# Performance work log

Measured on AMD Instinct MI355X. Metric: run time of the kernel, lower is better.

Reference implementation:

```python
import jax, jax.numpy as jnp
import numpy as np

DIM = 1024
HEADS = 16
MLP = 4096

def setup_inputs() -> dict:
    key = jax.random.key(0)
    ks = jax.random.split(key, 8)
    s = 0.02
    return {
        "x": jax.random.normal(ks[0], (4, 2048, DIM), dtype=jnp.float32),
        "W_qkv": jax.random.normal(ks[1], (DIM, 3 * DIM), dtype=jnp.float32) * s,
        "W_o": jax.random.normal(ks[2], (DIM, DIM), dtype=jnp.float32) * s,
        "b_o": jnp.zeros((DIM,), dtype=jnp.float32),
        "g1": jnp.ones((DIM,), dtype=jnp.float32),
        "be1": jnp.zeros((DIM,), dtype=jnp.float32),
        "W1": jax.random.normal(ks[3], (DIM, MLP), dtype=jnp.float32) * s,
        "b1": jnp.zeros((MLP,), dtype=jnp.float32),
        "W2": jax.random.normal(ks[4], (MLP, DIM), dtype=jnp.float32) * s,
        "b2": jnp.zeros((DIM,), dtype=jnp.float32),
        "g2": jnp.ones((DIM,), dtype=jnp.float32),
        "be2": jnp.zeros((DIM,), dtype=jnp.float32),
    }

def _gelu(x):
    # GELU approx used in source: x * sigmoid(1.702 * x)
    return x * jax.nn.sigmoid(1.702 * x)

def _layernorm(x, g, b, eps=1e-5):
    mu = jnp.mean(x, axis=-1, keepdims=True)
    var = jnp.var(x, axis=-1, keepdims=True)
    return (x - mu) * jax.lax.rsqrt(var + eps) * g + b

def reference(x, W_qkv, W_o, b_o, g1, be1, W1, b1, W2, b2, g2, be2):
    b, n, d = x.shape
    h = HEADS
    hd = d // h
    scale = hd ** -0.5
    qkv = x @ W_qkv                               # [b,n,3d]
    q, k, v = jnp.split(qkv, 3, axis=-1)
    q = q.reshape(b, n, h, hd).transpose(0, 2, 1, 3)  # [b,h,n,hd]
    k = k.reshape(b, n, h, hd).transpose(0, 2, 1, 3)
    v = v.reshape(b, n, h, hd).transpose(0, 2, 1, 3)
    dots = jnp.einsum('bhid,bhjd->bhij', q, k) * scale  # [b,h,n,n]
    attn = jax.nn.softmax(dots, axis=-1)
    out = jnp.einsum('bhij,bhjd->bhid', attn, v)
    out = out.transpose(0, 2, 1, 3).reshape(b, n, d)
    out = out @ W_o + b_o
    x = _layernorm(x + out, g1, be1)
    ff = _gelu(x @ W1 + b1) @ W2 + b2
    x = _layernorm(x + ff, g2, be2)
    return x
```

## Files before the change

kernel.cpp:

```cpp
#include <hip/hip_runtime.h>

typedef unsigned short u16;
typedef __attribute__((ext_vector_type(4))) float f32x4;
typedef __attribute__((ext_vector_type(8))) __bf16 bf16x8;
typedef __attribute__((ext_vector_type(8))) unsigned short u16x8;
typedef __attribute__((ext_vector_type(4))) unsigned short u16x4;

__device__ __forceinline__ u16 f2bf(float f) {
  __bf16 h = (__bf16)f;
  union { __bf16 h; u16 u; } v; v.h = h;
  return v.u;
}

__device__ __forceinline__ void async16(const void* g, void* l) {
  __builtin_amdgcn_global_load_lds(
      (const __attribute__((address_space(1))) unsigned int*)g,
      (__attribute__((address_space(3))) unsigned int*)l, 16, 0, 0);
}

__device__ __forceinline__ void barrier_f() {
  asm volatile("" ::: "memory");
  __builtin_amdgcn_s_barrier();
  asm volatile("" ::: "memory");
}

__global__ __launch_bounds__(256) void cvt_f32_bf16(const float* __restrict__ in,
                                                    u16* __restrict__ out, int n4) {
  int i = blockIdx.x * 256 + threadIdx.x;
  if (i >= n4) return;
  f32x4 v = *(const f32x4*)(in + (long)i * 4);
  u16x4 o;
#pragma unroll
  for (int j = 0; j < 4; j++) o[j] = f2bf(v[j]);
  *(u16x4*)(out + (long)i * 4) = o;
}

__global__ __launch_bounds__(256) void transpose_cvt(const float* __restrict__ W,
                                                     u16* __restrict__ Wt, int K, int N) {
  __shared__ float tile[32][33];
  int n0 = blockIdx.x * 32, k0 = blockIdx.y * 32;
  int tx = threadIdx.x & 31, ty = threadIdx.x >> 5;
#pragma unroll
  for (int i = 0; i < 32; i += 8)
    tile[ty + i][tx] = W[(long)(k0 + ty + i) * N + n0 + tx];
  __syncthreads();
#pragma unroll
  for (int i = 0; i < 32; i += 8)
    Wt[(long)(n0 + ty + i) * K + k0 + tx] = f2bf(tile[tx][ty + i]);
}

__global__ __launch_bounds__(256) void vtrans(const u16* __restrict__ qkv,
                                              u16* __restrict__ vt) {
  const int bh = blockIdx.y, kt = blockIdx.x * 64;
  const int b = bh >> 4, h = bh & 15;
  const long tok0 = (long)b * 2048;
  const int t = threadIdx.x;
  const int r = t >> 3, c8 = (t & 7) * 8;
  u16x8 v0 = *(const u16x8*)&qkv[(tok0 + kt + r) * 3072 + 2048 + h * 64 + c8];
  u16x8 v1 = *(const u16x8*)&qkv[(tok0 + kt + r + 32) * 3072 + 2048 + h * 64 + c8];
#pragma unroll
  for (int j = 0; j < 8; j++) {
    vt[((long)bh * 64 + c8 + j) * 2048 + kt + r] = v0[j];
    vt[((long)bh * 64 + c8 + j) * 2048 + kt + r + 32] = v1[j];
  }
}

template <int BIAS, int GELU, int OBF, int QSCALE>
__global__ __launch_bounds__(512, 1) void gemm8p(const u16* __restrict__ A,
                                                 const u16* __restrict__ Bt,
                                                 void* __restrict__ Cp,
                                                 const float* __restrict__ bias,
                                                 int M, int N, int K) {
  __shared__ u16 As[2][256 * 64];
  __shared__ u16 Bs[2][256 * 64];
  const int t = threadIdx.x, wid = t >> 6, ln = t & 63;
  const int lr = ln & 15, lg = ln >> 4;
  const int wr = wid >> 2, wc = wid & 3;

  const int nwg = gridDim.x * gridDim.y;
  const int flat = blockIdx.y * gridDim.x + blockIdx.x;
  const int cpx = nwg >> 3;
  const int swz = (flat & 7) * cpx + (flat >> 3);
  const int m0 = (swz / gridDim.x) * 256, n0 = (swz % gridDim.x) * 256;
  const int NT = K >> 6;

  const int srow = t >> 3;
  const int sch = ((t & 7) ^ (srow & 7)) * 8;
  const u16* gA = A + (long)(m0 + srow) * K + sch;
  const u16* gB = Bt + (long)(n0 + srow) * K + sch;
  const long KL = K;

#define STAGE_A(tt, h)                                                     \
  {                                                                        \
    const u16* s_ = gA + (long)((h) * 128) * KL + (long)(tt) * 64;         \
    char* d_ = (char*)As + ((tt) & 1) * 32768 + (h) * 16384 + wid * 1024;  \
    async16(s_, d_);                                                       \
    async16(s_ + 64 * KL, d_ + 8192);                                      \
  }
#define STAGE_B(tt, h)                                                     \
  {                                                                        \
    const u16* s_ = gB + (long)((h) * 128) * KL + (long)(tt) * 64;         \
    char* d_ = (char*)Bs + ((tt) & 1) * 32768 + (h) * 16384 + wid * 1024;  \
    async16(s_, d_);                                                       \
    async16(s_ + 64 * KL, d_ + 8192);                                      \
  }

  f32x4 acc[8][4] = {};
  const int cx0 = (lg ^ (lr & 7)) * 16;
  const int cx1 = ((4 + lg) ^ (lr & 7)) * 16;

  STAGE_A(0, 0); STAGE_A(0, 1);
  STAGE_B(0, 0); STAGE_B(0, 1);
  STAGE_A(1, 0); STAGE_A(1, 1);

  for (int tK = 0; tK < NT; ++tK) {
    const int cur = tK & 1;
    const char* ldsA = (const char*)As + cur * 32768;
    const char* ldsB = (const char*)Bs + cur * 32768;
    if (tK == NT - 1) {
      asm volatile("s_waitcnt vmcnt(0)" ::: "memory");
    } else {
      asm volatile("s_waitcnt vmcnt(4)" ::: "memory");
    }
    barrier_f();

    bf16x8 aLo[4][2], aHi[4][2], bLo[2][2], bHi[2][2];
#pragma unroll
    for (int mf = 0; mf < 4; mf++) {
      int row = wr * 128 + mf * 16 + lr;
      aLo[mf][0] = *(const bf16x8*)(ldsA + row * 128 + cx0);
      aLo[mf][1] = *(const bf16x8*)(ldsA + row * 128 + cx1);
    }
#pragma unroll
    for (int nf = 0; nf < 2; nf++) {
      int row = wc * 64 + nf * 16 + lr;
      bLo[nf][0] = *(const bf16x8*)(ldsB + row * 128 + cx0);
      bLo[nf][1] = *(const bf16x8*)(ldsB + row * 128 + cx1);
    }
    if (tK + 1 < NT) STAGE_B(tK + 1, 0);
    barrier_f();
    __builtin_amdgcn_s_setprio(1);
#pragma unroll
    for (int mf = 0; mf < 4; mf++)
#pragma unroll
      for (int nf = 0; nf < 2; nf++) {
        acc[mf][nf] = __builtin_amdgcn_mfma_f32_16x16x32_bf16(aLo[mf][0], bLo[nf][0], acc[mf][nf], 0, 0, 0);
        acc[mf][nf] = __builtin_amdgcn_mfma_f32_16x16x32_bf16(aLo[mf][1], bLo[nf][1], acc[mf][nf], 0, 0, 0);
      }
    __builtin_amdgcn_s_setprio(0);
    barrier_f();

#pragma unroll
    for (int mf = 0; mf < 4; mf++) {
      int row = wr * 128 + (mf + 4) * 16 + lr;
      aHi[mf][0] = *(const bf16x8*)(ldsA + row * 128 + cx0);
      aHi[mf][1] = *(const bf16x8*)(ldsA + row * 128 + cx1);
    }
    if (tK + 1 < NT) STAGE_B(tK + 1, 1);
    barrier_f();
    __builtin_amdgcn_s_setprio(1);
#pragma unroll
    for (int mf = 0; mf < 4; mf++)
#pragma unroll
      for (int nf = 0; nf < 2; nf++) {
        acc[mf + 4][nf] = __builtin_amdgcn_mfma_f32_16x16x32_bf16(aHi[mf][0], bLo[nf][0], acc[mf + 4][nf], 0, 0, 0);
        acc[mf + 4][nf] = __builtin_amdgcn_mfma_f32_16x16x32_bf16(aHi[mf][1], bLo[nf][1], acc[mf + 4][nf], 0, 0, 0);
      }
    __builtin_amdgcn_s_setprio(0);
    barrier_f();

#pragma unroll
    for (int nf = 0; nf < 2; nf++) {
      int row = wc * 64 + (nf + 2) * 16 + lr;
      bHi[nf][0] = *(const bf16x8*)(ldsB + row * 128 + cx0);
      bHi[nf][1] = *(const bf16x8*)(ldsB + row * 128 + cx1);
    }
    if (tK + 2 < NT) STAGE_A(tK + 2, 0);
    barrier_f();
    __builtin_amdgcn_s_setprio(1);
#pragma unroll
    for (int mf = 0; mf < 4; mf++)
#pragma unroll
      for (int nf = 0; nf < 2; nf++) {
        acc[mf][nf + 2] = __builtin_amdgcn_mfma_f32_16x16x32_bf16(aLo[mf][0], bHi[nf][0], acc[mf][nf + 2], 0, 0, 0);
        acc[mf][nf + 2] = __builtin_amdgcn_mfma_f32_16x16x32_bf16(aLo[mf][1], bHi[nf][1], acc[mf][nf + 2], 0, 0, 0);
      }
    __builtin_amdgcn_s_setprio(0);
    barrier_f();

    if (tK + 2 < NT) STAGE_A(tK + 2, 1);
    barrier_f();
    __builtin_amdgcn_s_setprio(1);
#pragma unroll
    for (int mf = 0; mf < 4; mf++)
#pragma unroll
      for (int nf = 0; nf < 2; nf++) {
        acc[mf + 4][nf + 2] = __builtin_amdgcn_mfma_f32_16x16x32_bf16(aHi[mf][0], bHi[nf][0], acc[mf + 4][nf + 2], 0, 0, 0);
        acc[mf + 4][nf + 2] = __builtin_amdgcn_mfma_f32_16x16x32_bf16(aHi[mf][1], bHi[nf][1], acc[mf + 4][nf + 2], 0, 0, 0);
      }
    __builtin_amdgcn_s_setprio(0);
    barrier_f();
  }
#undef STAGE_A
#undef STAGE_B

#pragma unroll
  for (int mf = 0; mf < 8; mf++) {
    int rbase = m0 + wr * 128 + mf * 16 + lg * 4;
#pragma unroll
    for (int nf = 0; nf < 4; nf++) {
      int col = n0 + wc * 64 + nf * 16 + lr;
      float bv = BIAS ? bias[col] : 0.f;
#pragma unroll
      for (int r = 0; r < 4; r++) {
        float v = acc[mf][nf][r] + bv;
        if (GELU) v = v / (1.f + __expf(-1.702f * v));
        if (QSCALE && col < 1024) v *= 0.18033688011112043f;
        if (OBF) ((u16*)Cp)[(long)(rbase + r) * N + col] = f2bf(v);
        else ((float*)Cp)[(long)(rbase + r) * N + col] = v;
      }
    }
  }
}

template <int BIAS, int GELU, int OBF, int QSCALE>
__global__ __launch_bounds__(256, 2) void gemm128(const u16* __restrict__ A,
                                                  const u16* __restrict__ Bt,
                                                  void* __restrict__ Cp,
                                                  const float* __restrict__ bias,
                                                  int M, int N, int K) {
  __shared__ u16 As[128 * 32];
  __shared__ u16 Bs[128 * 32];
  const int t = threadIdx.x, ln = t & 63, wv = t >> 6;
  const int wr = wv >> 1, wc = wv & 1;
  const int lr = ln & 15, lg = ln >> 4;
  const int m0 = blockIdx.y * 128, n0 = blockIdx.x * 128;

  const u16* gA = A + (long)(m0 + (t >> 2)) * K + (t & 3) * 8;
  const u16* gA2 = gA + (long)64 * K;
  const u16* gB = Bt + (long)(n0 + (t >> 2)) * K + (t & 3) * 8;
  const u16* gB2 = gB + (long)64 * K;
  char* ldsA = (char*)As + wv * 1024;
  char* ldsB = (char*)Bs + wv * 1024;

  f32x4 acc[4][4] = {};

  for (int kt = 0; kt < K; kt += 32) {
    __syncthreads();
    async16(gA, ldsA);
    async16(gA2, ldsA + 4096);
    async16(gB, ldsB);
    async16(gB2, ldsB + 4096);
    gA += 32; gA2 += 32; gB += 32; gB2 += 32;
    __syncthreads();
    bf16x8 aF[4], bF[4];
#pragma unroll
    for (int i = 0; i < 4; i++) {
      aF[i] = *(const bf16x8*)&As[(wr * 64 + i * 16 + lr) * 32 + lg * 8];
      bF[i] = *(const bf16x8*)&Bs[(wc * 64 + i * 16 + lr) * 32 + lg * 8];
    }
#pragma unroll
    for (int i = 0; i < 4; i++)
#pragma unroll
      for (int j = 0; j < 4; j++)
        acc[i][j] = __builtin_amdgcn_mfma_f32_16x16x32_bf16(aF[i], bF[j], acc[i][j], 0, 0, 0);
  }

#pragma unroll
  for (int i = 0; i < 4; i++) {
    int rbase = m0 + wr * 64 + i * 16 + lg * 4;
#pragma unroll
    for (int j = 0; j < 4; j++) {
      int col = n0 + wc * 64 + j * 16 + lr;
      float bv = BIAS ? bias[col] : 0.f;
#pragma unroll
      for (int r = 0; r < 4; r++) {
        float v = acc[i][j][r] + bv;
        if (GELU) v = v / (1.f + __expf(-1.702f * v));
        if (QSCALE && col < 1024) v *= 0.18033688011112043f;
        if (OBF) ((u16*)Cp)[(long)(rbase + r) * N + col] = f2bf(v);
        else ((float*)Cp)[(long)(rbase + r) * N + col] = v;
      }
    }
  }
}

__global__ __launch_bounds__(512, 6) void attn_kernel(const u16* __restrict__ qkv,
                                                      const u16* __restrict__ vt,
                                                      u16* __restrict__ out) {
  const int b = blockIdx.y >> 4, h = blockIdx.y & 15;
  const int q0 = blockIdx.x * 128;
  const int t = threadIdx.x, wv = t >> 6, ln = t & 63;
  const int lr = ln & 15, lg = ln >> 4;
  __shared__ u16 Ks[2][64 * 64];
  __shared__ u16 Vs[2][64 * 64];
  __shared__ u16 Pl[8][16 * 64];
  const long tok0 = (long)b * 2048;

  bf16x8 aQ[2];
  {
    long row = tok0 + q0 + wv * 16 + lr;
#pragma unroll
    for (int kf = 0; kf < 2; kf++)
      aQ[kf] = *(const bf16x8*)&qkv[row * 3072 + h * 64 + kf * 32 + lg * 8];
  }

  const int isK = (t < 256);
  const int tt = t & 255;
  const int sr = tt >> 3;
  const int sc = ((tt & 7) ^ (sr & 7)) * 8;
  const u16* gS = isK ? qkv + (tok0 + sr) * 3072 + 1024 + h * 64 + sc
                      : vt + ((long)(b * 16 + h) * 64 + sr) * 2048 + sc;
  const long src2 = isK ? (long)32 * 3072 : (long)32 * 2048;
  const long step = isK ? (long)64 * 3072 : 64;
  char* const dS = (isK ? (char*)&Ks[0][0] : (char*)&Vs[0][0]) + (wv & 3) * 1024;

  float m_i = -1e30f;
  f32x4 accO[4] = {};
  f32x4 accL = {};

  bf16x8 bOnes;
  {
    union { u16x8 u; bf16x8 b; } ou;
#pragma unroll
    for (int j = 0; j < 8; j++) ou.u[j] = 0x3F80;
    bOnes = ou.b;
  }

  async16(gS, dS);
  async16(gS + src2, dS + 4096);
  const u16* gSn = gS + step;

  for (int it = 0; it < 32; ++it) {
    const int cur = it & 1;
    if (it < 31) {
      char* nS = dS + (cur ^ 1) * 8192;
      async16(gSn, nS);
      async16(gSn + src2, nS + 4096);
      gSn += step;
      asm volatile("s_waitcnt vmcnt(2)" ::: "memory");
    } else {
      asm volatile("s_waitcnt vmcnt(0)" ::: "memory");
    }
    __builtin_amdgcn_s_barrier();
    __builtin_amdgcn_sched_barrier(0);
    const u16* Kc = &Ks[cur][0];
    const u16* Vc = &Vs[cur][0];

    f32x4 accS[4];
    __builtin_amdgcn_s_setprio(1);
#pragma unroll
    for (int nc = 0; nc < 4; nc++) {
      f32x4 s = {};
#pragma unroll
      for (int kf = 0; kf < 2; kf++) {
        int krow = nc * 16 + lr;
        bf16x8 aK = *(const bf16x8*)&Kc[krow * 64 + ((kf * 32 + lg * 8) ^ ((krow & 7) << 3))];
        s = __builtin_amdgcn_mfma_f32_16x16x32_bf16(aK, aQ[kf], s, 0, 0, 0);
      }
      accS[nc] = s;
    }
    __builtin_amdgcn_s_setprio(0);

    float tm = fmaxf(fmaxf(accS[0][0], accS[0][1]), accS[0][2]);
    tm = fmaxf(fmaxf(tm, accS[0][3]), accS[1][0]);
    tm = fmaxf(fmaxf(tm, accS[1][1]), accS[1][2]);
    tm = fmaxf(fmaxf(tm, accS[1][3]), accS[2][0]);
    tm = fmaxf(fmaxf(tm, accS[2][1]), accS[2][2]);
    tm = fmaxf(fmaxf(tm, accS[2][3]), accS[3][0]);
    tm = fmaxf(fmaxf(tm, accS[3][1]), accS[3][2]);
    tm = fmaxf(tm, accS[3][3]);
    tm = fmaxf(tm, __shfl_xor(tm, 16));
    tm = fmaxf(tm, __shfl_xor(tm, 32));

    if (!__all(tm <= m_i + 11.0f)) {
      float mn = fmaxf(m_i, tm);
      float corr = exp2f(m_i - mn);
      m_i = mn;
      float cb[4];
#pragma unroll
      for (int j = 0; j < 4; j++) cb[j] = __shfl(corr, lg * 4 + j);
#pragma unroll
      for (int d = 0; d < 4; d++)
#pragma unroll
        for (int j = 0; j < 4; j++) accO[d][j] *= cb[j];
#pragma unroll
      for (int j = 0; j < 4; j++) accL[j] *= cb[j];
    }

    u16x4 pw[4];
#pragma unroll
    for (int nc = 0; nc < 4; nc++) {
#pragma unroll
      for (int r = 0; r < 4; r++) pw[nc][r] = f2bf(exp2f(accS[nc][r] - m_i));
    }
#pragma unroll
    for (int nc = 0; nc < 4; nc++)
      *(u16x4*)&Pl[wv][lr * 64 + ((nc * 16 + lg * 4) ^ ((lr & 7) << 3))] = pw[nc];

    __builtin_amdgcn_s_setprio(1);
#pragma unroll
    for (int kf = 0; kf < 2; kf++) {
      bf16x8 aP = *(const bf16x8*)&Pl[wv][lr * 64 + ((kf * 32 + lg * 8) ^ ((lr & 7) << 3))];
      accL = __builtin_amdgcn_mfma_f32_16x16x32_bf16(aP, bOnes, accL, 0, 0, 0);
#pragma unroll
      for (int d = 0; d < 4; d++) {
        int vrow = d * 16 + lr;
        bf16x8 bV = *(const bf16x8*)&Vc[vrow * 64 + ((kf * 32 + lg * 8) ^ ((vrow & 7) << 3))];
        accO[d] = __builtin_amdgcn_mfma_f32_16x16x32_bf16(aP, bV, accO[d], 0, 0, 0);
      }
    }
    __builtin_amdgcn_s_setprio(0);
    __builtin_amdgcn_s_barrier();
    __builtin_amdgcn_sched_barrier(0);
  }

  float inv[4];
#pragma unroll
  for (int j = 0; j < 4; j++) inv[j] = 1.f / accL[j];
#pragma unroll
  for (int d = 0; d < 4; d++) {
#pragma unroll
    for (int j = 0; j < 4; j++) {
      float v = accO[d][j] * inv[j];
      out[(tok0 + q0 + wv * 16 + lg * 4 + j) * 1024 + h * 64 + d * 16 + lr] = f2bf(v);
    }
  }
}

template <int WB>
__global__ __launch_bounds__(256) void ln_kernel(const float* __restrict__ xin,
                                                 const float* __restrict__ res,
                                                 const float* __restrict__ g,
                                                 const float* __restrict__ be,
                                                 float* __restrict__ of,
                                                 u16* __restrict__ ob) {
  int row = blockIdx.x, t = threadIdx.x;
  long base = (long)row * 1024 + t * 4;
  f32x4 a = *(const f32x4*)(xin + base);
  f32x4 bv = *(const f32x4*)(res + base);
  f32x4 v = a + bv;
  float s = v[0] + v[1] + v[2] + v[3];
  float ss = v[0] * v[0] + v[1] * v[1] + v[2] * v[2] + v[3] * v[3];
#pragma unroll
  for (int o = 1; o < 64; o <<= 1) { s += __shfl_xor(s, o); ss += __shfl_xor(ss, o); }
  __shared__ float sm[8];
  if ((t & 63) == 0) { sm[t >> 6] = s; sm[4 + (t >> 6)] = ss; }
  __syncthreads();
  s = sm[0] + sm[1] + sm[2] + sm[3];
  ss = sm[4] + sm[5] + sm[6] + sm[7];
  float mu = s * 0.0009765625f;
  float var = ss * 0.0009765625f - mu * mu;
  float inv = rsqrtf(var + 1e-5f);
  f32x4 gg = *(const f32x4*)(g + t * 4);
  f32x4 bb = *(const f32x4*)(be + t * 4);
  f32x4 y;
#pragma unroll
  for (int j = 0; j < 4; j++) y[j] = (v[j] - mu) * inv * gg[j] + bb[j];
  *(f32x4*)(of + base) = y;
  if (WB) {
    u16x4 o4;
#pragma unroll
    for (int j = 0; j < 4; j++) o4[j] = f2bf(y[j]);
    *(u16x4*)(ob + base) = o4;
  }
}

extern "C" void kernel_launch(void* const* d_in, const int* in_sizes, int n_in,
                              void* d_out, int out_size, void* d_ws, size_t ws_size,
                              hipStream_t stream) {
  const float* x = (const float*)d_in[0];
  const float* Wqkv = (const float*)d_in[1];
  const float* Wo = (const float*)d_in[2];
  const float* bo = (const float*)d_in[3];
  const float* g1 = (const float*)d_in[4];
  const float* be1 = (const float*)d_in[5];
  const float* W1 = (const float*)d_in[6];
  const float* b1 = (const float*)d_in[7];
  const float* W2 = (const float*)d_in[8];
  const float* b2 = (const float*)d_in[9];
  const float* g2 = (const float*)d_in[10];
  const float* be2 = (const float*)d_in[11];
  float* out = (float*)d_out;
  char* ws = (char*)d_ws;

  u16* xb = (u16*)(ws + 0);
  u16* qkvb = (u16*)(ws + 16777216);
  u16* h1b = (u16*)(ws + 0);
  u16* attnb = (u16*)(ws + 67108864);
  u16* vtb = (u16*)(ws + 83886080);
  float* proj = (float*)(ws + 83886080);
  float* ff = (float*)(ws + 67108864);
  float* x1f = (float*)(ws + 117440512);
  u16* x1b = (u16*)(ws + 150994944);
  u16* wqkvt = (u16*)(ws + 167772160);
  u16* wot = (u16*)(ws + 174063616);
  u16* w1t = (u16*)(ws + 176160768);
  u16* w2t = (u16*)(ws + 184549376);

  cvt_f32_bf16<<<8192, 256, 0, stream>>>(x, xb, 2097152);
  transpose_cvt<<<dim3(96, 32), 256, 0, stream>>>(Wqkv, wqkvt, 1024, 3072);
  transpose_cvt<<<dim3(32, 32), 256, 0, stream>>>(Wo, wot, 1024, 1024);
  transpose_cvt<<<dim3(128, 32), 256, 0, stream>>>(W1, w1t, 1024, 4096);
  transpose_cvt<<<dim3(32, 128), 256, 0, stream>>>(W2, w2t, 4096, 1024);
  gemm8p<0, 0, 1, 1><<<dim3(12, 32), 512, 0, stream>>>(xb, wqkvt, qkvb, nullptr, 8192, 3072, 1024);
  vtrans<<<dim3(32, 64), 256, 0, stream>>>(qkvb, vtb);
  attn_kernel<<<dim3(16, 64), 512, 0, stream>>>(qkvb, vtb, attnb);
  gemm128<1, 0, 0, 0><<<dim3(8, 64), 256, 0, stream>>>(attnb, wot, proj, bo, 8192, 1024, 1024);
  ln_kernel<1><<<8192, 256, 0, stream>>>(x, proj, g1, be1, x1f, x1b);
  gemm8p<1, 1, 1, 0><<<dim3(16, 32), 512, 0, stream>>>(x1b, w1t, h1b, b1, 8192, 4096, 1024);
  gemm128<1, 0, 0, 0><<<dim3(8, 64), 256, 0, stream>>>(h1b, w2t, ff, b2, 8192, 1024, 4096);
  ln_kernel<0><<<8192, 256, 0, stream>>>(x1f, ff, g2, be2, out, nullptr);
}
```

Before: 467.3 us.

## Fuse V transpose into QKV GEMM epilogue and split-K the FFN down-projection

```diff
diff --git a/kernel.cpp b/kernel.cpp
--- a/kernel.cpp
+++ b/kernel.cpp
@@ -49,46 +49,35 @@
     Wt[(long)(n0 + ty + i) * K + k0 + tx] = f2bf(tile[tx][ty + i]);
 }
 
-__global__ __launch_bounds__(256) void vtrans(const u16* __restrict__ qkv,
-                                              u16* __restrict__ vt) {
-  const int bh = blockIdx.y, kt = blockIdx.x * 64;
-  const int b = bh >> 4, h = bh & 15;
-  const long tok0 = (long)b * 2048;
-  const int t = threadIdx.x;
-  const int r = t >> 3, c8 = (t & 7) * 8;
-  u16x8 v0 = *(const u16x8*)&qkv[(tok0 + kt + r) * 3072 + 2048 + h * 64 + c8];
-  u16x8 v1 = *(const u16x8*)&qkv[(tok0 + kt + r + 32) * 3072 + 2048 + h * 64 + c8];
-#pragma unroll
-  for (int j = 0; j < 8; j++) {
-    vt[((long)bh * 64 + c8 + j) * 2048 + kt + r] = v0[j];
-    vt[((long)bh * 64 + c8 + j) * 2048 + kt + r + 32] = v1[j];
-  }
-}
-
-template <int BIAS, int GELU, int OBF, int QSCALE>
+template <int BIAS, int GELU, int OBF, int QSCALE, int VW>
 __global__ __launch_bounds__(512, 1) void gemm8p(const u16* __restrict__ A,
                                                  const u16* __restrict__ Bt,
                                                  void* __restrict__ Cp,
                                                  const float* __restrict__ bias,
-                                                 int M, int N, int K) {
+                                                 u16* __restrict__ vt,
+                                                 int M, int N, int Kst, int Klen) {
   __shared__ u16 As[2][256 * 64];
   __shared__ u16 Bs[2][256 * 64];
   const int t = threadIdx.x, wid = t >> 6, ln = t & 63;
   const int lr = ln & 15, lg = ln >> 4;
   const int wr = wid >> 2, wc = wid & 3;
 
-  const int nwg = gridDim.x * gridDim.y;
-  const int flat = blockIdx.y * gridDim.x + blockIdx.x;
+  const int gx = gridDim.x, gy = gridDim.y;
+  const int nwg = gx * gy * gridDim.z;
+  const int flat = (blockIdx.z * gy + blockIdx.y) * gx + blockIdx.x;
   const int cpx = nwg >> 3;
   const int swz = (flat & 7) * cpx + (flat >> 3);
-  const int m0 = (swz / gridDim.x) * 256, n0 = (swz % gridDim.x) * 256;
-  const int NT = K >> 6;
+  const int sx = swz % gx, rest = swz / gx;
+  const int sy = rest % gy, sz = rest / gy;
+  const int m0 = sy * 256, n0 = sx * 256;
+  const long zo = (long)sz * Klen;
+  const int NT = Klen >> 6;
 
   const int srow = t >> 3;
   const int sch = ((t & 7) ^ (srow & 7)) * 8;
-  const u16* gA = A + (long)(m0 + srow) * K + sch;
-  const u16* gB = Bt + (long)(n0 + srow) * K + sch;
-  const long KL = K;
+  const u16* gA = A + (long)(m0 + srow) * Kst + zo + sch;
+  const u16* gB = Bt + (long)(n0 + srow) * Kst + zo + sch;
+  const long KL = Kst;
 
 #define STAGE_A(tt, h)                                                     \
   {                                                                        \
@@ -204,6 +193,7 @@
 #undef STAGE_A
 #undef STAGE_B
 
+  float* const Cf = (float*)Cp + (long)sz * M * N;
 #pragma unroll
   for (int mf = 0; mf < 8; mf++) {
     int rbase = m0 + wr * 128 + mf * 16 + lg * 4;
@@ -211,13 +201,22 @@
     for (int nf = 0; nf < 4; nf++) {
       int col = n0 + wc * 64 + nf * 16 + lr;
       float bv = BIAS ? bias[col] : 0.f;
-#pragma unroll
-      for (int r = 0; r < 4; r++) {
-        float v = acc[mf][nf][r] + bv;
-        if (GELU) v = v / (1.f + __expf(-1.702f * v));
-        if (QSCALE && col < 1024) v *= 0.18033688011112043f;
-        if (OBF) ((u16*)Cp)[(long)(rbase + r) * N + col] = f2bf(v);
-        else ((float*)Cp)[(long)(rbase + r) * N + col] = v;
+      if (VW && col >= 2048) {
+        int hd = col - 2048;
+        int bq = rbase >> 11, key = rbase & 2047;
+        u16x4 o4;
+#pragma unroll
+        for (int r = 0; r < 4; r++) o4[r] = f2bf(acc[mf][nf][r]);
+        *(u16x4*)&vt[((long)(bq * 16 + (hd >> 6)) * 64 + (hd & 63)) * 2048 + key] = o4;
+      } else {
+#pragma unroll
+        for (int r = 0; r < 4; r++) {
+          float v = acc[mf][nf][r] + bv;
+          if (GELU) v = v / (1.f + __expf(-1.702f * v));
+          if (QSCALE && col < 1024) v *= 0.18033688011112043f;
+          if (OBF) ((u16*)Cp)[(long)(rbase + r) * N + col] = f2bf(v);
+          else Cf[(long)(rbase + r) * N + col] = v;
+        }
       }
     }
   }
@@ -428,9 +427,11 @@
   }
 }
 
-template <int WB>
+template <int WB, int R2>
 __global__ __launch_bounds__(256) void ln_kernel(const float* __restrict__ xin,
                                                  const float* __restrict__ res,
+                                                 const float* __restrict__ res2,
+                                                 const float* __restrict__ bias,
                                                  const float* __restrict__ g,
                                                  const float* __restrict__ be,
                                                  float* __restrict__ of,
@@ -440,6 +441,11 @@
   f32x4 a = *(const f32x4*)(xin + base);
   f32x4 bv = *(const f32x4*)(res + base);
   f32x4 v = a + bv;
+  if (R2) {
+    f32x4 c = *(const f32x4*)(res2 + base);
+    f32x4 bb4 = *(const f32x4*)(bias + t * 4);
+    v = v + c + bb4;
+  }
   float s = v[0] + v[1] + v[2] + v[3];
   float ss = v[0] * v[0] + v[1] * v[1] + v[2] * v[2] + v[3] * v[3];
 #pragma unroll
@@ -487,15 +493,15 @@
   u16* xb = (u16*)(ws + 0);
   u16* qkvb = (u16*)(ws + 16777216);
   u16* h1b = (u16*)(ws + 0);
-  u16* attnb = (u16*)(ws + 67108864);
-  u16* vtb = (u16*)(ws + 83886080);
-  float* proj = (float*)(ws + 83886080);
-  float* ff = (float*)(ws + 67108864);
-  float* x1f = (float*)(ws + 117440512);
-  u16* x1b = (u16*)(ws + 150994944);
-  u16* wqkvt = (u16*)(ws + 167772160);
-  u16* wot = (u16*)(ws + 174063616);
-  u16* w1t = (u16*)(ws + 176160768);
+  u16* vtb = (u16*)(ws + 67108864);
+  u16* x1b = (u16*)(ws + 67108864);
+  u16* attnb = (u16*)(ws + 83886080);
+  float* x1f = (float*)(ws + 83886080);
+  float* projf = (float*)(ws + 117440512);
+  float* pf = (float*)(ws + 117440512);
+  u16* wqkvt = (u16*)(ws + 150994944);
+  u16* wot = (u16*)(ws + 157286400);
+  u16* w1t = (u16*)(ws + 159383552);
   u16* w2t = (u16*)(ws + 184549376);
 
   cvt_f32_bf16<<<8192, 256, 0, stream>>>(x, xb, 2097152);
@@ -503,12 +509,14 @@
   transpose_cvt<<<dim3(32, 32), 256, 0, stream>>>(Wo, wot, 1024, 1024);
   transpose_cvt<<<dim3(128, 32), 256, 0, stream>>>(W1, w1t, 1024, 4096);
   transpose_cvt<<<dim3(32, 128), 256, 0, stream>>>(W2, w2t, 4096, 1024);
-  gemm8p<0, 0, 1, 1><<<dim3(12, 32), 512, 0, stream>>>(xb, wqkvt, qkvb, nullptr, 8192, 3072, 1024);
-  vtrans<<<dim3(32, 64), 256, 0, stream>>>(qkvb, vtb);
+  gemm8p<0, 0, 1, 1, 1><<<dim3(12, 32, 1), 512, 0, stream>>>(
+      xb, wqkvt, qkvb, nullptr, vtb, 8192, 3072, 1024, 1024);
   attn_kernel<<<dim3(16, 64), 512, 0, stream>>>(qkvb, vtb, attnb);
-  gemm128<1, 0, 0, 0><<<dim3(8, 64), 256, 0, stream>>>(attnb, wot, proj, bo, 8192, 1024, 1024);
-  ln_kernel<1><<<8192, 256, 0, stream>>>(x, proj, g1, be1, x1f, x1b);
-  gemm8p<1, 1, 1, 0><<<dim3(16, 32), 512, 0, stream>>>(x1b, w1t, h1b, b1, 8192, 4096, 1024);
-  gemm128<1, 0, 0, 0><<<dim3(8, 64), 256, 0, stream>>>(h1b, w2t, ff, b2, 8192, 1024, 4096);
-  ln_kernel<0><<<8192, 256, 0, stream>>>(x1f, ff, g2, be2, out, nullptr);
-}
+  gemm128<1, 0, 0, 0><<<dim3(8, 64), 256, 0, stream>>>(attnb, wot, projf, bo, 8192, 1024, 1024);
+  ln_kernel<1, 0><<<8192, 256, 0, stream>>>(x, projf, nullptr, nullptr, g1, be1, x1f, x1b);
+  gemm8p<1, 1, 1, 0, 0><<<dim3(16, 32, 1), 512, 0, stream>>>(
+      x1b, w1t, h1b, b1, nullptr, 8192, 4096, 1024, 1024);
+  gemm8p<0, 0, 0, 0, 0><<<dim3(4, 32, 2), 512, 0, stream>>>(
+      h1b, w2t, pf, nullptr, nullptr, 8192, 1024, 4096, 2048);
+  ln_kernel<0, 1><<<8192, 256, 0, stream>>>(x1f, pf, pf + (long)8192 * 1024, b2, g2, be2, out, nullptr);
+}
```

Result: faster. 428.6 us (-8.3%).
